# Performance work log

Hardware: AMD Instinct MI355X
Metric: run time of the kernel (lower is better)

The kernel has to match this reference:

```python
import jax, jax.numpy as jnp
import numpy as np

DT = 0.01          # integration timestep
TH_HI = 1.0        # upper firing threshold
TH_LO = -1.0       # lower firing threshold


def setup_inputs() -> dict:
    key = jax.random.key(0)
    inputs = jax.random.normal(key, (64, 256, 1024), dtype=jnp.float32)
    return {"inputs": inputs}


def reference(inputs):
    # inputs: [B, T, D] pre-activation drive at each timestep
    rates = jnp.tanh(inputs)                     # activation(inputs), [B, T, D]
    x = jnp.swapaxes(rates, 0, 1)                # [T, B, D] for scan over time

    def step(v, r):
        v = v + r * DT                           # integrate
        sp = (v >= TH_HI).astype(v.dtype)        # positive spike
        sn = (v <= TH_LO).astype(v.dtype)        # negative spike
        v = v - sp * TH_HI - sn * TH_LO          # subtractive (self-regulating) reset
        out = (sp - sn) / DT                     # signed spike train scaled by 1/dt
        return v, out

    v0 = jnp.zeros(x.shape[1:], dtype=x.dtype)   # initial membrane state
    _, spikes = jax.lax.scan(step, v0, x)        # spikes: [T, B, D]
    spikes = jnp.swapaxes(spikes, 0, 1)          # [B, T, D]

    # spiking-aware (straight-through) output: spikes forward, rates gradient
    out = rates + jax.lax.stop_gradient(spikes - rates)
    return out
```

## Files before the change

kernel.cpp:

```cpp
#include <hip/hip_runtime.h>
#include <stdint.h>

#define B_DIM 64
#define T_STEPS 256
#define D_DIM 1024
#define TPB 256
#define SEQ_PER_BLK 64
#define TQ 64

__device__ __forceinline__ float xla_tanhf(float x) {
    const float kClamp = 7.90531110763549805f;
    float xc = fminf(fmaxf(x, -kClamp), kClamp);
    float x2 = xc * xc;
    float p = __builtin_fmaf(x2, -2.76076847742355e-16f, 2.00018790482477e-13f);
    p = __builtin_fmaf(x2, p, -8.60467152213735e-11f);
    p = __builtin_fmaf(x2, p, 5.12229709037114e-08f);
    p = __builtin_fmaf(x2, p, 1.48572235717979e-05f);
    p = __builtin_fmaf(x2, p, 6.37261928875436e-04f);
    p = __builtin_fmaf(x2, p, 4.89352455891786e-03f);
    p = xc * p;
    float q = __builtin_fmaf(x2, 1.19825839466702e-06f, 1.18534705686654e-04f);
    q = __builtin_fmaf(x2, q, 2.26843463243900e-03f);
    q = __builtin_fmaf(x2, q, 4.89352518554385e-03f);
    float r = p / q;
    return (fabsf(x) < 0.0004f) ? x : r;
}

#define LD(i) "global_load_dword %" #i ", %16, %17\n\t" \
              "v_add_u32 %16, 0x1000, %16\n\t"

#define ISSUE16(B) asm volatile( \
    LD(0) LD(1) LD(2) LD(3) LD(4) LD(5) LD(6) LD(7) \
    LD(8) LD(9) LD(10) LD(11) LD(12) LD(13) LD(14) LD(15) \
    : "=v"(B[0]), "=v"(B[1]), "=v"(B[2]), "=v"(B[3]), \
      "=v"(B[4]), "=v"(B[5]), "=v"(B[6]), "=v"(B[7]), \
      "=v"(B[8]), "=v"(B[9]), "=v"(B[10]), "=v"(B[11]), \
      "=v"(B[12]), "=v"(B[13]), "=v"(B[14]), "=v"(B[15]), \
      "+v"(voffi) \
    : "s"(inp_u) : "memory")

#define WAITBUF(B, CNT) asm volatile("s_waitcnt vmcnt(" CNT ")" \
    : "+v"(B[0]), "+v"(B[1]), "+v"(B[2]), "+v"(B[3]), \
      "+v"(B[4]), "+v"(B[5]), "+v"(B[6]), "+v"(B[7]), \
      "+v"(B[8]), "+v"(B[9]), "+v"(B[10]), "+v"(B[11]), \
      "+v"(B[12]), "+v"(B[13]), "+v"(B[14]), "+v"(B[15]) \
    :: "memory")

#define KEEP16(B) asm volatile("" \
    : "+v"(B[0]), "+v"(B[1]), "+v"(B[2]), "+v"(B[3]), \
      "+v"(B[4]), "+v"(B[5]), "+v"(B[6]), "+v"(B[7]), \
      "+v"(B[8]), "+v"(B[9]), "+v"(B[10]), "+v"(B[11]), \
      "+v"(B[12]), "+v"(B[13]), "+v"(B[14]), "+v"(B[15]))

#define TANH16(B) do { \
    _Pragma("unroll") \
    for (int u = 0; u < 16; ++u) B[u] = xla_tanhf(B[u]); \
    KEEP16(B); } while (0)

#define SCAN16(B) do { \
    _Pragma("unroll") \
    for (int u = 0; u < 16; ++u) { \
        float r = B[u]; \
        v = __builtin_fmaf(r, 0.01f, v); \
        float sp = (v >= 1.0f)  ? 1.0f : 0.0f; \
        float sn = (v <= -1.0f) ? 1.0f : 0.0f; \
        v = (v - sp) + sn; \
        B[u] = (sp - sn) * 100.0f; \
    } } while (0)

#define STORE16(B) asm volatile( \
    "global_store_dword %0, %1, %17\n\t"  "v_add_u32 %0, 0x1000, %0\n\t" \
    "global_store_dword %0, %2, %17\n\t"  "v_add_u32 %0, 0x1000, %0\n\t" \
    "global_store_dword %0, %3, %17\n\t"  "v_add_u32 %0, 0x1000, %0\n\t" \
    "global_store_dword %0, %4, %17\n\t"  "v_add_u32 %0, 0x1000, %0\n\t" \
    "global_store_dword %0, %5, %17\n\t"  "v_add_u32 %0, 0x1000, %0\n\t" \
    "global_store_dword %0, %6, %17\n\t"  "v_add_u32 %0, 0x1000, %0\n\t" \
    "global_store_dword %0, %7, %17\n\t"  "v_add_u32 %0, 0x1000, %0\n\t" \
    "global_store_dword %0, %8, %17\n\t"  "v_add_u32 %0, 0x1000, %0\n\t" \
    "global_store_dword %0, %9, %17\n\t"  "v_add_u32 %0, 0x1000, %0\n\t" \
    "global_store_dword %0, %10, %17\n\t" "v_add_u32 %0, 0x1000, %0\n\t" \
    "global_store_dword %0, %11, %17\n\t" "v_add_u32 %0, 0x1000, %0\n\t" \
    "global_store_dword %0, %12, %17\n\t" "v_add_u32 %0, 0x1000, %0\n\t" \
    "global_store_dword %0, %13, %17\n\t" "v_add_u32 %0, 0x1000, %0\n\t" \
    "global_store_dword %0, %14, %17\n\t" "v_add_u32 %0, 0x1000, %0\n\t" \
    "global_store_dword %0, %15, %17\n\t" "v_add_u32 %0, 0x1000, %0\n\t" \
    "global_store_dword %0, %16, %17\n\t" "v_add_u32 %0, 0x1000, %0\n\t" \
    : "+v"(voffo) \
    : "v"(B[0]), "v"(B[1]), "v"(B[2]), "v"(B[3]), \
      "v"(B[4]), "v"(B[5]), "v"(B[6]), "v"(B[7]), \
      "v"(B[8]), "v"(B[9]), "v"(B[10]), "v"(B[11]), \
      "v"(B[12]), "v"(B[13]), "v"(B[14]), "v"(B[15]), "s"(outp_u) \
    : "memory")

__global__ __launch_bounds__(TPB)
void spike_scan_kernel(const float* __restrict__ in, float* __restrict__ out) {
    __shared__ float vstate[3][SEQ_PER_BLK];
    __shared__ unsigned int flag[4];

    const int lane = threadIdx.x & 63;
    const int wk   = threadIdx.x >> 6;

    const uint32_t sgrp  = (uint32_t)blockIdx.x << 6;
    const uint32_t b     = sgrp >> 10;
    const uint32_t dbase = sgrp & (D_DIM - 1);
    uint32_t voffi = b * (T_STEPS * D_DIM * 4u)
                   + (uint32_t)wk * (TQ * D_DIM * 4u)
                   + (dbase + (uint32_t)lane) * 4u;
    uint32_t voffo = voffi;
    const uint64_t inp_u  = (uint64_t)in;
    const uint64_t outp_u = (uint64_t)out;

    float rA[16], rB[16], rC[16], rD[16];

    ISSUE16(rA); ISSUE16(rB); ISSUE16(rC); ISSUE16(rD);

    if (threadIdx.x < 4) flag[threadIdx.x] = 0u;
    asm volatile("s_waitcnt lgkmcnt(0)" ::: "memory");
    __builtin_amdgcn_s_barrier();

    WAITBUF(rA, "48"); TANH16(rA);
    WAITBUF(rB, "32"); TANH16(rB);
    WAITBUF(rC, "16"); TANH16(rC);
    WAITBUF(rD, "0");  TANH16(rD);

    float v = 0.0f;
    if (wk != 0) {
        while (__hip_atomic_load(&flag[wk - 1], __ATOMIC_ACQUIRE,
                                 __HIP_MEMORY_SCOPE_WORKGROUP) == 0u)
            __builtin_amdgcn_s_sleep(1);
        v = vstate[wk - 1][lane];
    }
    if (wk != 3) {
        SCAN16(rA); SCAN16(rB); SCAN16(rC); SCAN16(rD);
        vstate[wk][lane] = v;
        __hip_atomic_store(&flag[wk], 1u, __ATOMIC_RELEASE,
                           __HIP_MEMORY_SCOPE_WORKGROUP);
        STORE16(rA); STORE16(rB); STORE16(rC); STORE16(rD);
    } else {
        SCAN16(rA); STORE16(rA);
        SCAN16(rB); STORE16(rB);
        SCAN16(rC); STORE16(rC);
        SCAN16(rD); STORE16(rD);
    }
}

extern "C" void kernel_launch(void* const* d_in, const int* in_sizes, int n_in,
                              void* d_out, int out_size, void* d_ws, size_t ws_size,
                              hipStream_t stream) {
    const float* in = (const float*)d_in[0];
    float* out = (float*)d_out;
    dim3 block(TPB);
    dim3 grid((B_DIM * D_DIM) / SEQ_PER_BLK);
    spike_scan_kernel<<<grid, block, 0, stream>>>(in, out);
}
```

Baseline: 116.0 us.

## Process two channels per lane with dwordx2 loads and nontemporal stores

Each lane now handles two adjacent D channels, using 64-bit global loads and stores, so a block covers 128 sequences and the grid is halved. Output stores use the nt (nontemporal) hint, launch bounds request two blocks per CU, and the flag init barrier moves before the loads. The last wave no longer interleaves scan and store per buffer. Doubling the register buffers (128 VGPRs of data per thread) raises register pressure and may lower occupancy.

```diff
diff --git a/kernel.cpp b/kernel.cpp
--- a/kernel.cpp
+++ b/kernel.cpp
@@ -5,8 +5,10 @@
 #define T_STEPS 256
 #define D_DIM 1024
 #define TPB 256
-#define SEQ_PER_BLK 64
+#define SEQ_PER_BLK 128
 #define TQ 64
+
+typedef float f32x2 __attribute__((ext_vector_type(2)));
 
 __device__ __forceinline__ float xla_tanhf(float x) {
     const float kClamp = 7.90531110763549805f;
@@ -26,7 +28,7 @@
     return (fabsf(x) < 0.0004f) ? x : r;
 }
 
-#define LD(i) "global_load_dword %" #i ", %16, %17\n\t" \
+#define LD(i) "global_load_dwordx2 %" #i ", %16, %17\n\t" \
               "v_add_u32 %16, 0x1000, %16\n\t"
 
 #define ISSUE16(B) asm volatile( \
@@ -54,37 +56,46 @@
 
 #define TANH16(B) do { \
     _Pragma("unroll") \
-    for (int u = 0; u < 16; ++u) B[u] = xla_tanhf(B[u]); \
+    for (int u = 0; u < 16; ++u) { \
+        B[u].x = xla_tanhf(B[u].x); \
+        B[u].y = xla_tanhf(B[u].y); \
+    } \
     KEEP16(B); } while (0)
 
 #define SCAN16(B) do { \
     _Pragma("unroll") \
     for (int u = 0; u < 16; ++u) { \
-        float r = B[u]; \
-        v = __builtin_fmaf(r, 0.01f, v); \
-        float sp = (v >= 1.0f)  ? 1.0f : 0.0f; \
-        float sn = (v <= -1.0f) ? 1.0f : 0.0f; \
-        v = (v - sp) + sn; \
-        B[u] = (sp - sn) * 100.0f; \
+        float r0 = B[u].x; \
+        v0 = __builtin_fmaf(r0, 0.01f, v0); \
+        float sp0 = (v0 >= 1.0f)  ? 1.0f : 0.0f; \
+        float sn0 = (v0 <= -1.0f) ? 1.0f : 0.0f; \
+        v0 = (v0 - sp0) + sn0; \
+        B[u].x = (sp0 - sn0) * 100.0f; \
+        float r1 = B[u].y; \
+        v1 = __builtin_fmaf(r1, 0.01f, v1); \
+        float sp1 = (v1 >= 1.0f)  ? 1.0f : 0.0f; \
+        float sn1 = (v1 <= -1.0f) ? 1.0f : 0.0f; \
+        v1 = (v1 - sp1) + sn1; \
+        B[u].y = (sp1 - sn1) * 100.0f; \
     } } while (0)
 
 #define STORE16(B) asm volatile( \
-    "global_store_dword %0, %1, %17\n\t"  "v_add_u32 %0, 0x1000, %0\n\t" \
-    "global_store_dword %0, %2, %17\n\t"  "v_add_u32 %0, 0x1000, %0\n\t" \
-    "global_store_dword %0, %3, %17\n\t"  "v_add_u32 %0, 0x1000, %0\n\t" \
-    "global_store_dword %0, %4, %17\n\t"  "v_add_u32 %0, 0x1000, %0\n\t" \
-    "global_store_dword %0, %5, %17\n\t"  "v_add_u32 %0, 0x1000, %0\n\t" \
-    "global_store_dword %0, %6, %17\n\t"  "v_add_u32 %0, 0x1000, %0\n\t" \
-    "global_store_dword %0, %7, %17\n\t"  "v_add_u32 %0, 0x1000, %0\n\t" \
-    "global_store_dword %0, %8, %17\n\t"  "v_add_u32 %0, 0x1000, %0\n\t" \
-    "global_store_dword %0, %9, %17\n\t"  "v_add_u32 %0, 0x1000, %0\n\t" \
-    "global_store_dword %0, %10, %17\n\t" "v_add_u32 %0, 0x1000, %0\n\t" \
-    "global_store_dword %0, %11, %17\n\t" "v_add_u32 %0, 0x1000, %0\n\t" \
-    "global_store_dword %0, %12, %17\n\t" "v_add_u32 %0, 0x1000, %0\n\t" \
-    "global_store_dword %0, %13, %17\n\t" "v_add_u32 %0, 0x1000, %0\n\t" \
-    "global_store_dword %0, %14, %17\n\t" "v_add_u32 %0, 0x1000, %0\n\t" \
-    "global_store_dword %0, %15, %17\n\t" "v_add_u32 %0, 0x1000, %0\n\t" \
-    "global_store_dword %0, %16, %17\n\t" "v_add_u32 %0, 0x1000, %0\n\t" \
+    "global_store_dwordx2 %0, %1, %17 nt\n\t"  "v_add_u32 %0, 0x1000, %0\n\t" \
+    "global_store_dwordx2 %0, %2, %17 nt\n\t"  "v_add_u32 %0, 0x1000, %0\n\t" \
+    "global_store_dwordx2 %0, %3, %17 nt\n\t"  "v_add_u32 %0, 0x1000, %0\n\t" \
+    "global_store_dwordx2 %0, %4, %17 nt\n\t"  "v_add_u32 %0, 0x1000, %0\n\t" \
+    "global_store_dwordx2 %0, %5, %17 nt\n\t"  "v_add_u32 %0, 0x1000, %0\n\t" \
+    "global_store_dwordx2 %0, %6, %17 nt\n\t"  "v_add_u32 %0, 0x1000, %0\n\t" \
+    "global_store_dwordx2 %0, %7, %17 nt\n\t"  "v_add_u32 %0, 0x1000, %0\n\t" \
+    "global_store_dwordx2 %0, %8, %17 nt\n\t"  "v_add_u32 %0, 0x1000, %0\n\t" \
+    "global_store_dwordx2 %0, %9, %17 nt\n\t"  "v_add_u32 %0, 0x1000, %0\n\t" \
+    "global_store_dwordx2 %0, %10, %17 nt\n\t" "v_add_u32 %0, 0x1000, %0\n\t" \
+    "global_store_dwordx2 %0, %11, %17 nt\n\t" "v_add_u32 %0, 0x1000, %0\n\t" \
+    "global_store_dwordx2 %0, %12, %17 nt\n\t" "v_add_u32 %0, 0x1000, %0\n\t" \
+    "global_store_dwordx2 %0, %13, %17 nt\n\t" "v_add_u32 %0, 0x1000, %0\n\t" \
+    "global_store_dwordx2 %0, %14, %17 nt\n\t" "v_add_u32 %0, 0x1000, %0\n\t" \
+    "global_store_dwordx2 %0, %15, %17 nt\n\t" "v_add_u32 %0, 0x1000, %0\n\t" \
+    "global_store_dwordx2 %0, %16, %17 nt\n\t" "v_add_u32 %0, 0x1000, %0\n\t" \
     : "+v"(voffo) \
     : "v"(B[0]), "v"(B[1]), "v"(B[2]), "v"(B[3]), \
       "v"(B[4]), "v"(B[5]), "v"(B[6]), "v"(B[7]), \
@@ -92,7 +103,7 @@
       "v"(B[12]), "v"(B[13]), "v"(B[14]), "v"(B[15]), "s"(outp_u) \
     : "memory")
 
-__global__ __launch_bounds__(TPB)
+__global__ __launch_bounds__(TPB, 2)
 void spike_scan_kernel(const float* __restrict__ in, float* __restrict__ out) {
     __shared__ float vstate[3][SEQ_PER_BLK];
     __shared__ unsigned int flag[4];
@@ -100,48 +111,44 @@
     const int lane = threadIdx.x & 63;
     const int wk   = threadIdx.x >> 6;
 
-    const uint32_t sgrp  = (uint32_t)blockIdx.x << 6;
+    if (threadIdx.x < 4) flag[threadIdx.x] = 0u;
+    __syncthreads();
+
+    const uint32_t sgrp  = (uint32_t)blockIdx.x * SEQ_PER_BLK;
     const uint32_t b     = sgrp >> 10;
     const uint32_t dbase = sgrp & (D_DIM - 1);
     uint32_t voffi = b * (T_STEPS * D_DIM * 4u)
                    + (uint32_t)wk * (TQ * D_DIM * 4u)
-                   + (dbase + (uint32_t)lane) * 4u;
+                   + (dbase + 2u * (uint32_t)lane) * 4u;
     uint32_t voffo = voffi;
     const uint64_t inp_u  = (uint64_t)in;
     const uint64_t outp_u = (uint64_t)out;
 
-    float rA[16], rB[16], rC[16], rD[16];
+    f32x2 rA[16], rB[16], rC[16], rD[16];
 
     ISSUE16(rA); ISSUE16(rB); ISSUE16(rC); ISSUE16(rD);
-
-    if (threadIdx.x < 4) flag[threadIdx.x] = 0u;
-    asm volatile("s_waitcnt lgkmcnt(0)" ::: "memory");
-    __builtin_amdgcn_s_barrier();
-
     WAITBUF(rA, "48"); TANH16(rA);
     WAITBUF(rB, "32"); TANH16(rB);
     WAITBUF(rC, "16"); TANH16(rC);
     WAITBUF(rD, "0");  TANH16(rD);
 
-    float v = 0.0f;
+    float v0 = 0.0f, v1 = 0.0f;
     if (wk != 0) {
         while (__hip_atomic_load(&flag[wk - 1], __ATOMIC_ACQUIRE,
                                  __HIP_MEMORY_SCOPE_WORKGROUP) == 0u)
             __builtin_amdgcn_s_sleep(1);
-        v = vstate[wk - 1][lane];
+        v0 = vstate[wk - 1][2 * lane];
+        v1 = vstate[wk - 1][2 * lane + 1];
     }
+    SCAN16(rA); SCAN16(rB); SCAN16(rC); SCAN16(rD);
     if (wk != 3) {
-        SCAN16(rA); SCAN16(rB); SCAN16(rC); SCAN16(rD);
-        vstate[wk][lane] = v;
+        vstate[wk][2 * lane]     = v0;
+        vstate[wk][2 * lane + 1] = v1;
         __hip_atomic_store(&flag[wk], 1u, __ATOMIC_RELEASE,
                            __HIP_MEMORY_SCOPE_WORKGROUP);
-        STORE16(rA); STORE16(rB); STORE16(rC); STORE16(rD);
-    } else {
-        SCAN16(rA); STORE16(rA);
-        SCAN16(rB); STORE16(rB);
-        SCAN16(rC); STORE16(rC);
-        SCAN16(rD); STORE16(rD);
     }
+
+    STORE16(rA); STORE16(rB); STORE16(rC); STORE16(rD);
 }
 
 extern "C" void kernel_launch(void* const* d_in, const int* in_sizes, int n_in,
```

Result: slower. 120.3 us (+3.7%).
